# Kernel tuning notes

Measured on AMD Instinct MI355X. Metric: run time of the kernel, lower is better.

The kernel has to match this reference:

```python
import jax, jax.numpy as jnp
import numpy as np

IN_FEATURES = 8192
OUT_FEATURES = 8192
MAX_STATES = 100
THRESHOLD = float(MAX_STATES // 2)  # 50.0


def setup_inputs() -> dict:
    key = jax.random.key(0)
    k1, k2, k3, k4 = jax.random.split(key, 4)
    spike_input = (jax.random.uniform(k1, (1, IN_FEATURES)) < 0.2).astype(jnp.float32)  # sparse binary spikes
    synapse_states = jax.random.uniform(k2, (OUT_FEATURES, IN_FEATURES)) * MAX_STATES  # straddles THRESHOLD
    membrane_potential = jax.random.uniform(k3, (OUT_FEATURES,)) * 3.0
    adaptive_threshold = jnp.full((OUT_FEATURES,), 3.0, dtype=jnp.float32)
    eligibility_trace = jax.random.uniform(k4, (OUT_FEATURES, IN_FEATURES)) * 3.0
    return {
        "spike_input": spike_input,
        "synapse_states": synapse_states,
        "membrane_potential": membrane_potential,
        "adaptive_threshold": adaptive_threshold,
        "eligibility_trace": eligibility_trace,
    }


def reference(spike_input, synapse_states, membrane_potential, adaptive_threshold, eligibility_trace):
    # Ternary (here effectively binary 0/1) weight generation from synapse states
    w = (synapse_states > THRESHOLD).astype(jnp.float32)  # [O, I]
    x = spike_input.reshape(1, -1)                        # [1, I]
    current = (x @ w.T).reshape(-1)                       # [O]

    # LIF membrane update: v <- 0.6*v + I
    v = membrane_potential * 0.6 + current                # [O]
    spikes = (v >= adaptive_threshold).astype(jnp.float32)  # [O]

    # Hebbian eligibility trace: decay, add outer-product, clamp
    trace_new = jnp.clip(
        eligibility_trace * 0.7 + jnp.outer(spikes, x.reshape(-1)),
        0.0, 3.0,
    )  # [O, I]

    # Soft reset of membrane potential where a spike occurred
    v_new = v * (1.0 - spikes) * 0.3                      # [O]

    return spikes, v_new, trace_new
```

## Files before the change

### kernel.cpp

```cpp
#include <hip/hip_runtime.h>


#define IN_F 8192
#define OUT_F 8192
#define SYN_THRESH 50.0f

__global__ __launch_bounds__(256) void snn_fused_kernel(
    const float* __restrict__ x,
    const float* __restrict__ syn,
    const float* __restrict__ mp,
    const float* __restrict__ thr,
    const float* __restrict__ trace,
    float* __restrict__ out_spikes,
    float* __restrict__ out_vnew,
    float* __restrict__ out_trace)
{
    const int row = blockIdx.x;
    const int tid = threadIdx.x;
    const long long base = (long long)row * IN_F;

    const float4* __restrict__ x4   = (const float4*)x;
    const float4* __restrict__ syn4 = (const float4*)(syn + base);
    const float4* __restrict__ tr4  = (const float4*)(trace + base);
    float4* __restrict__ ot4        = (float4*)(out_trace + base);

    float4 xv[8];
    float sum = 0.0f;
#pragma unroll
    for (int j = 0; j < 8; ++j) {
        const int idx = j * 256 + tid;
        xv[j] = x4[idx];
        const float4 s = syn4[idx];
        sum += ((s.x > SYN_THRESH) ? xv[j].x : 0.0f)
             + ((s.y > SYN_THRESH) ? xv[j].y : 0.0f)
             + ((s.z > SYN_THRESH) ? xv[j].z : 0.0f)
             + ((s.w > SYN_THRESH) ? xv[j].w : 0.0f);
    }

#pragma unroll
    for (int off = 32; off > 0; off >>= 1)
        sum += __shfl_down(sum, off, 64);

    __shared__ float wave_sums[4];
    __shared__ float s_spike;
    const int wave = tid >> 6;
    if ((tid & 63) == 0) wave_sums[wave] = sum;
    __syncthreads();

    if (tid == 0) {
        const float current = wave_sums[0] + wave_sums[1] + wave_sums[2] + wave_sums[3];
        const float v = mp[row] * 0.6f + current;
        const float spike = (v >= thr[row]) ? 1.0f : 0.0f;
        out_spikes[row] = spike;
        out_vnew[row]   = v * (1.0f - spike) * 0.3f;
        s_spike = spike;
    }
    __syncthreads();
    const float spike = s_spike;

#pragma unroll
    for (int j = 0; j < 8; ++j) {
        const int idx = j * 256 + tid;
        float4 t = tr4[idx];
        t.x = fminf(fmaxf(t.x * 0.7f + spike * xv[j].x, 0.0f), 3.0f);
        t.y = fminf(fmaxf(t.y * 0.7f + spike * xv[j].y, 0.0f), 3.0f);
        t.z = fminf(fmaxf(t.z * 0.7f + spike * xv[j].z, 0.0f), 3.0f);
        t.w = fminf(fmaxf(t.w * 0.7f + spike * xv[j].w, 0.0f), 3.0f);
        ot4[idx] = t;
    }
}

extern "C" void kernel_launch(void* const* d_in, const int* in_sizes, int n_in,
                              void* d_out, int out_size, void* d_ws, size_t ws_size,
                              hipStream_t stream) {
    const float* x     = (const float*)d_in[0];
    const float* syn   = (const float*)d_in[1];
    const float* mp    = (const float*)d_in[2];
    const float* thr   = (const float*)d_in[3];
    const float* trace = (const float*)d_in[4];

    float* out = (float*)d_out;
    float* out_spikes = out;
    float* out_vnew   = out + OUT_F;
    float* out_trace  = out + 2 * OUT_F;

    snn_fused_kernel<<<OUT_F, 256, 0, stream>>>(
        x, syn, mp, thr, trace, out_spikes, out_vnew, out_trace);
}
```

Before: 583.1 us.

## Map one wavefront per output row, drop block syncs, use nontemporal trace stores

Each 64-lane wavefront now owns a full output row, so a 256-thread block handles four rows. The reduction stays within the wave using xor shuffles, which removes the shared-memory exchange and both __syncthreads barriers. The x vector is re-read in the trace loop instead of being held in registers, and the trace output is written with nontemporal stores to keep it from polluting cache. In exchange, each wave issues more serial loads per row (32 iterations instead of 8), and x is loaded twice.

```diff
diff --git a/kernel.cpp b/kernel.cpp
--- a/kernel.cpp
+++ b/kernel.cpp
@@ -5,7 +5,9 @@
 #define OUT_F 8192
 #define SYN_THRESH 50.0f
 
-__global__ __launch_bounds__(256) void snn_fused_kernel(
+typedef float vfloat4 __attribute__((ext_vector_type(4)));
+
+__global__ __launch_bounds__(256) void snn_fused_wave(
     const float* __restrict__ x,
     const float* __restrict__ syn,
     const float* __restrict__ mp,
@@ -15,58 +17,49 @@
     float* __restrict__ out_vnew,
     float* __restrict__ out_trace)
 {
-    const int row = blockIdx.x;
-    const int tid = threadIdx.x;
+    const int wave = threadIdx.x >> 6;
+    const int lane = threadIdx.x & 63;
+    const int row  = (blockIdx.x << 2) | wave;
     const long long base = (long long)row * IN_F;
 
-    const float4* __restrict__ x4   = (const float4*)x;
-    const float4* __restrict__ syn4 = (const float4*)(syn + base);
-    const float4* __restrict__ tr4  = (const float4*)(trace + base);
-    float4* __restrict__ ot4        = (float4*)(out_trace + base);
+    const vfloat4* __restrict__ x4   = (const vfloat4*)x;
+    const vfloat4* __restrict__ syn4 = (const vfloat4*)(syn + base);
+    const vfloat4* __restrict__ tr4  = (const vfloat4*)(trace + base);
+    vfloat4* __restrict__ ot4        = (vfloat4*)(out_trace + base);
 
-    float4 xv[8];
     float sum = 0.0f;
 #pragma unroll
-    for (int j = 0; j < 8; ++j) {
-        const int idx = j * 256 + tid;
-        xv[j] = x4[idx];
-        const float4 s = syn4[idx];
-        sum += ((s.x > SYN_THRESH) ? xv[j].x : 0.0f)
-             + ((s.y > SYN_THRESH) ? xv[j].y : 0.0f)
-             + ((s.z > SYN_THRESH) ? xv[j].z : 0.0f)
-             + ((s.w > SYN_THRESH) ? xv[j].w : 0.0f);
+    for (int j = 0; j < 32; ++j) {
+        const int idx = (j << 6) | lane;
+        const vfloat4 s  = syn4[idx];
+        const vfloat4 xx = x4[idx];
+        sum += ((s.x > SYN_THRESH) ? xx.x : 0.0f)
+             + ((s.y > SYN_THRESH) ? xx.y : 0.0f)
+             + ((s.z > SYN_THRESH) ? xx.z : 0.0f)
+             + ((s.w > SYN_THRESH) ? xx.w : 0.0f);
     }
 
 #pragma unroll
     for (int off = 32; off > 0; off >>= 1)
-        sum += __shfl_down(sum, off, 64);
+        sum += __shfl_xor(sum, off, 64);
 
-    __shared__ float wave_sums[4];
-    __shared__ float s_spike;
-    const int wave = tid >> 6;
-    if ((tid & 63) == 0) wave_sums[wave] = sum;
-    __syncthreads();
-
-    if (tid == 0) {
-        const float current = wave_sums[0] + wave_sums[1] + wave_sums[2] + wave_sums[3];
-        const float v = mp[row] * 0.6f + current;
-        const float spike = (v >= thr[row]) ? 1.0f : 0.0f;
+    const float v     = mp[row] * 0.6f + sum;
+    const float spike = (v >= thr[row]) ? 1.0f : 0.0f;
+    if (lane == 0) {
         out_spikes[row] = spike;
         out_vnew[row]   = v * (1.0f - spike) * 0.3f;
-        s_spike = spike;
     }
-    __syncthreads();
-    const float spike = s_spike;
 
 #pragma unroll
-    for (int j = 0; j < 8; ++j) {
-        const int idx = j * 256 + tid;
-        float4 t = tr4[idx];
-        t.x = fminf(fmaxf(t.x * 0.7f + spike * xv[j].x, 0.0f), 3.0f);
-        t.y = fminf(fmaxf(t.y * 0.7f + spike * xv[j].y, 0.0f), 3.0f);
-        t.z = fminf(fmaxf(t.z * 0.7f + spike * xv[j].z, 0.0f), 3.0f);
-        t.w = fminf(fmaxf(t.w * 0.7f + spike * xv[j].w, 0.0f), 3.0f);
-        ot4[idx] = t;
+    for (int j = 0; j < 32; ++j) {
+        const int idx = (j << 6) | lane;
+        vfloat4 t        = tr4[idx];
+        const vfloat4 xx = x4[idx];
+        t.x = fminf(fmaxf(fmaf(t.x, 0.7f, spike * xx.x), 0.0f), 3.0f);
+        t.y = fminf(fmaxf(fmaf(t.y, 0.7f, spike * xx.y), 0.0f), 3.0f);
+        t.z = fminf(fmaxf(fmaf(t.z, 0.7f, spike * xx.z), 0.0f), 3.0f);
+        t.w = fminf(fmaxf(fmaf(t.w, 0.7f, spike * xx.w), 0.0f), 3.0f);
+        __builtin_nontemporal_store(t, &ot4[idx]);
     }
 }
 
@@ -84,6 +77,6 @@
     float* out_vnew   = out + OUT_F;
     float* out_trace  = out + 2 * OUT_F;
 
-    snn_fused_kernel<<<OUT_F, 256, 0, stream>>>(
+    snn_fused_wave<<<OUT_F / 4, 256, 0, stream>>>(
         x, syn, mp, thr, trace, out_spikes, out_vnew, out_trace);
 }
```

Result: no change. 589.8 us (+1.2%).
